# Kernel tuning notes

Measured on AMD Instinct MI355X. Metric: run time of the kernel, lower is better.

## Reference

```python
import jax, jax.numpy as jnp
import numpy as np

# 8-neighbor crop offsets in the exact order used by the torch module:
# (rows, cols) slices relative to the full image; center is [1:-1,1:-1]
_OFFSETS = [
    (slice(0, -2), slice(0, -2)),
    (slice(0, -2), slice(1, -1)),
    (slice(0, -2), slice(2, None)),
    (slice(1, -1), slice(0, -2)),
    (slice(2, None), slice(0, -2)),
    (slice(2, None), slice(1, -1)),
    (slice(2, None), slice(2, None)),
    (slice(1, -1), slice(2, None)),
]


def setup_inputs() -> dict:
    key = jax.random.key(0)
    k1, k2, k3 = jax.random.split(key, 3)
    x = jax.random.normal(k1, (32, 3, 256, 256), dtype=jnp.float32)
    w = jax.random.normal(k2, (3, 5, 8), dtype=jnp.float32)   # (in_ch, lbp_ch, 8)
    wl = jax.random.normal(k3, (5, 64), dtype=jnp.float32)    # (lbp_ch, out_ch)
    return {"x": x, "w": w, "wl": wl}


def reference(x, w, wl):
    # x: [n, i, H, W]; center crop [n, i, H-2, W-2]
    c = x[:, :, 1:-1, 1:-1]
    # 8 shifted sign-differences stacked on new axis l -> [n, i, 8, h, w]
    diffs = jnp.stack([jnp.sign(c - x[:, :, r, cc]) for (r, cc) in _OFFSETS], axis=2)
    # per-input-channel LBP mixing: [n,i,8,h,w] x exp(w)[i,m,8] -> [n,i,m,h,w]
    y = jnp.einsum('nilwh,iml->nimwh', diffs, jnp.exp(w))
    # sum over input channels i and project lbp channel m -> out channel o
    y = jnp.einsum('nimwh,mo->nowh', y, wl)
    # residual concat of cropped input, then zero-pad 1 on each spatial side
    out = jnp.concatenate([c, y], axis=1)
    return jnp.pad(out, ((0, 0), (0, 0), (1, 1), (1, 1)))
```

## Files before the change

kernel.cpp:

```cpp
#include <hip/hip_runtime.h>

#define HH 256
#define WW 256
#define HW (HH * WW)

__global__ void exp_kernel(const float* __restrict__ w, float* __restrict__ E) {
    int t = threadIdx.x;
    if (t < 120) E[t] = expf(w[t]);
}

__device__ __forceinline__ float sgnf(float d) {
    return (d > 0.0f) ? 1.0f : ((d < 0.0f) ? -1.0f : 0.0f);
}

__global__ __launch_bounds__(256) void lbp_kernel(
    const float* __restrict__ x,
    const float* __restrict__ E,
    const float* __restrict__ wl,
    float* __restrict__ out)
{
    const int tid = threadIdx.x;
    const int bid = blockIdx.x;
    const int n = bid >> 8;
    const int r = bid & 255;
    const int c = tid;

    float* ob = out + (size_t)n * 67 * HW + (size_t)r * WW + c;

    if (r == 0 || r == HH - 1 || c == 0 || c == WW - 1) {
        #pragma unroll
        for (int ch = 0; ch < 67; ++ch) ob[(size_t)ch * HW] = 0.0f;
        return;
    }

    const float* xb = x + (size_t)n * 3 * HW + (size_t)r * WW + c;

    float t[5] = {0.f, 0.f, 0.f, 0.f, 0.f};

    #pragma unroll
    for (int i = 0; i < 3; ++i) {
        const float* xp = xb + i * HW;
        const float ctr = xp[0];
        ob[i * HW] = ctr;

        float s[8];
        s[0] = sgnf(ctr - xp[-WW - 1]);
        s[1] = sgnf(ctr - xp[-WW    ]);
        s[2] = sgnf(ctr - xp[-WW + 1]);
        s[3] = sgnf(ctr - xp[-1]);
        s[4] = sgnf(ctr - xp[ WW - 1]);
        s[5] = sgnf(ctr - xp[ WW    ]);
        s[6] = sgnf(ctr - xp[ WW + 1]);
        s[7] = sgnf(ctr - xp[ 1]);

        #pragma unroll
        for (int m = 0; m < 5; ++m) {
            float acc = t[m];
            #pragma unroll
            for (int l = 0; l < 8; ++l)
                acc = fmaf(s[l], E[i * 40 + m * 8 + l], acc);
            t[m] = acc;
        }
    }

    #pragma unroll
    for (int o = 0; o < 64; ++o) {
        float v = t[0] * wl[o];
        #pragma unroll
        for (int m = 1; m < 5; ++m)
            v = fmaf(t[m], wl[m * 64 + o], v);
        ob[(size_t)(3 + o) * HW] = v;
    }
}

extern "C" void kernel_launch(void* const* d_in, const int* in_sizes, int n_in,
                              void* d_out, int out_size, void* d_ws, size_t ws_size,
                              hipStream_t stream) {
    const float* x  = (const float*)d_in[0];
    const float* w  = (const float*)d_in[1];
    const float* wl = (const float*)d_in[2];
    float* out = (float*)d_out;
    float* E   = (float*)d_ws;

    exp_kernel<<<1, 128, 0, stream>>>(w, E);
    lbp_kernel<<<32 * 256, 256, 0, stream>>>(x, E, wl, out);
}
```

Baseline: 622.0 us.

## Compute four columns per thread with float4 loads and stores

```diff
diff --git a/kernel.cpp b/kernel.cpp
--- a/kernel.cpp
+++ b/kernel.cpp
@@ -4,9 +4,15 @@
 #define WW 256
 #define HW (HH * WW)
 
-__global__ void exp_kernel(const float* __restrict__ w, float* __restrict__ E) {
+__global__ void prep_kernel(const float* __restrict__ w, const float* __restrict__ wl,
+                            float* __restrict__ ws) {
     int t = threadIdx.x;
-    if (t < 120) E[t] = expf(w[t]);
+    if (t < 120) ws[t] = expf(w[t]);
+    if (t >= 128 && t < 128 + 320) {
+        int idx = t - 128;
+        int o = idx / 5, m = idx - o * 5;
+        ws[t] = wl[m * 64 + o];
+    }
 }
 
 __device__ __forceinline__ float sgnf(float d) {
@@ -15,61 +21,111 @@
 
 __global__ __launch_bounds__(256) void lbp_kernel(
     const float* __restrict__ x,
-    const float* __restrict__ E,
-    const float* __restrict__ wl,
+    const float* __restrict__ ws,
     float* __restrict__ out)
 {
-    const int tid = threadIdx.x;
-    const int bid = blockIdx.x;
-    const int n = bid >> 8;
-    const int r = bid & 255;
-    const int c = tid;
+    const int tid  = threadIdx.x;
+    const int bid  = blockIdx.x;
+    const int n    = bid >> 6;
+    const int q    = bid & 63;
+    const int wv   = tid >> 6;
+    const int lane = tid & 63;
+    const int r    = q * 4 + wv;
+    const int cb   = lane * 4;
 
-    float* ob = out + (size_t)n * 67 * HW + (size_t)r * WW + c;
+    float* ob = out + (size_t)n * 67 * HW + (size_t)r * WW + cb;
 
-    if (r == 0 || r == HH - 1 || c == 0 || c == WW - 1) {
+    if (r == 0 || r == HH - 1) {
+        const float4 z = {0.f, 0.f, 0.f, 0.f};
         #pragma unroll
-        for (int ch = 0; ch < 67; ++ch) ob[(size_t)ch * HW] = 0.0f;
+        for (int ch = 0; ch < 67; ++ch)
+            *(float4*)(ob + (size_t)ch * HW) = z;
         return;
     }
 
-    const float* xb = x + (size_t)n * 3 * HW + (size_t)r * WW + c;
+    const int cl = (cb == 0) ? 0 : cb - 1;
+    const int cr = (cb + 4 > WW - 1) ? WW - 1 : cb + 4;
 
-    float t[5] = {0.f, 0.f, 0.f, 0.f, 0.f};
+    const float* xb = x + (size_t)n * 3 * HW + (size_t)r * WW;
+
+    float tacc[5][4];
+    #pragma unroll
+    for (int m = 0; m < 5; ++m)
+        #pragma unroll
+        for (int j = 0; j < 4; ++j) tacc[m][j] = 0.f;
 
     #pragma unroll
     for (int i = 0; i < 3; ++i) {
-        const float* xp = xb + i * HW;
-        const float ctr = xp[0];
-        ob[i * HW] = ctr;
+        const float* xr = xb + (size_t)i * HW;
 
-        float s[8];
-        s[0] = sgnf(ctr - xp[-WW - 1]);
-        s[1] = sgnf(ctr - xp[-WW    ]);
-        s[2] = sgnf(ctr - xp[-WW + 1]);
-        s[3] = sgnf(ctr - xp[-1]);
-        s[4] = sgnf(ctr - xp[ WW - 1]);
-        s[5] = sgnf(ctr - xp[ WW    ]);
-        s[6] = sgnf(ctr - xp[ WW + 1]);
-        s[7] = sgnf(ctr - xp[ 1]);
+        float4 m4 = *(const float4*)(xr - WW + cb);
+        float4 c4 = *(const float4*)(xr + cb);
+        float4 p4 = *(const float4*)(xr + WW + cb);
 
+        float rm[6], rc[6], rp[6];
+        rm[0] = xr[-WW + cl]; rm[1] = m4.x; rm[2] = m4.y; rm[3] = m4.z; rm[4] = m4.w; rm[5] = xr[-WW + cr];
+        rc[0] = xr[cl];       rc[1] = c4.x; rc[2] = c4.y; rc[3] = c4.z; rc[4] = c4.w; rc[5] = xr[cr];
+        rp[0] = xr[ WW + cl]; rp[1] = p4.x; rp[2] = p4.y; rp[3] = p4.z; rp[4] = p4.w; rp[5] = xr[ WW + cr];
+
+        float cv[4];
         #pragma unroll
-        for (int m = 0; m < 5; ++m) {
-            float acc = t[m];
+        for (int j = 0; j < 4; ++j) {
+            const float ctr = rc[j + 1];
+            cv[j] = ctr;
+            float s0 = sgnf(ctr - rm[j]);
+            float s1 = sgnf(ctr - rm[j + 1]);
+            float s2 = sgnf(ctr - rm[j + 2]);
+            float s3 = sgnf(ctr - rc[j]);
+            float s4 = sgnf(ctr - rp[j]);
+            float s5 = sgnf(ctr - rp[j + 1]);
+            float s6 = sgnf(ctr - rp[j + 2]);
+            float s7 = sgnf(ctr - rc[j + 2]);
+
             #pragma unroll
-            for (int l = 0; l < 8; ++l)
-                acc = fmaf(s[l], E[i * 40 + m * 8 + l], acc);
-            t[m] = acc;
+            for (int m = 0; m < 5; ++m) {
+                const float* Em = ws + i * 40 + m * 8;
+                float a = tacc[m][j];
+                a = fmaf(s0, Em[0], a);
+                a = fmaf(s1, Em[1], a);
+                a = fmaf(s2, Em[2], a);
+                a = fmaf(s3, Em[3], a);
+                a = fmaf(s4, Em[4], a);
+                a = fmaf(s5, Em[5], a);
+                a = fmaf(s6, Em[6], a);
+                a = fmaf(s7, Em[7], a);
+                tacc[m][j] = a;
+            }
+        }
+
+        float4 cc;
+        cc.x = (cb + 0 != 0 && cb + 0 != WW - 1) ? cv[0] : 0.f;
+        cc.y = cv[1];
+        cc.z = cv[2];
+        cc.w = (cb + 3 != WW - 1) ? cv[3] : 0.f;
+        *(float4*)(ob + (size_t)i * HW) = cc;
+    }
+
+    #pragma unroll
+    for (int j = 0; j < 4; ++j) {
+        const int col = cb + j;
+        if (col == 0 || col == WW - 1) {
+            #pragma unroll
+            for (int m = 0; m < 5; ++m) tacc[m][j] = 0.f;
         }
     }
 
+    const float* wlT = ws + 128;
+    float* yb = ob + (size_t)3 * HW;
     #pragma unroll
     for (int o = 0; o < 64; ++o) {
-        float v = t[0] * wl[o];
-        #pragma unroll
-        for (int m = 1; m < 5; ++m)
-            v = fmaf(t[m], wl[m * 64 + o], v);
-        ob[(size_t)(3 + o) * HW] = v;
+        const float* wo = wlT + o * 5;
+        const float w0 = wo[0], w1 = wo[1], w2 = wo[2], w3 = wo[3], w4 = wo[4];
+        float4 y;
+        y.x = fmaf(tacc[4][0], w4, fmaf(tacc[3][0], w3, fmaf(tacc[2][0], w2, fmaf(tacc[1][0], w1, tacc[0][0] * w0))));
+        y.y = fmaf(tacc[4][1], w4, fmaf(tacc[3][1], w3, fmaf(tacc[2][1], w2, fmaf(tacc[1][1], w1, tacc[0][1] * w0))));
+        y.z = fmaf(tacc[4][2], w4, fmaf(tacc[3][2], w3, fmaf(tacc[2][2], w2, fmaf(tacc[1][2], w1, tacc[0][2] * w0))));
+        y.w = fmaf(tacc[4][3], w4, fmaf(tacc[3][3], w3, fmaf(tacc[2][3], w2, fmaf(tacc[1][3], w1, tacc[0][3] * w0))));
+        *(float4*)(yb + (size_t)o * HW) = y;
     }
 }
 
@@ -80,8 +136,8 @@
     const float* w  = (const float*)d_in[1];
     const float* wl = (const float*)d_in[2];
     float* out = (float*)d_out;
-    float* E   = (float*)d_ws;
+    float* ws  = (float*)d_ws;
 
-    exp_kernel<<<1, 128, 0, stream>>>(w, E);
-    lbp_kernel<<<32 * 256, 256, 0, stream>>>(x, E, wl, out);
+    prep_kernel<<<1, 512, 0, stream>>>(w, wl, ws);
+    lbp_kernel<<<32 * 64, 256, 0, stream>>>(x, ws, out);
 }
```

After: 570.0 us. -8.4%, faster.
